# Optimization experiments

Measured on AMD Instinct MI355X. Metric: run time of the kernel, lower is better.

## Reference

```python
import jax, jax.numpy as jnp
import numpy as np

D_MODEL = 512
D_FF = 4 * D_MODEL
NUM_EXPERTS = 8
TOP_K = 2
NUM_TASKS = 16
D_TASK = 64
BATCH = 8
SEQ = 4096
LN_EPS = 1e-5


def setup_inputs() -> dict:
    key = jax.random.key(0)
    ks = jax.random.split(key, 10)
    s_in = 1.0 / np.sqrt(D_MODEL)
    s_ff = 1.0 / np.sqrt(D_FF)
    s_g = 1.0 / np.sqrt(D_MODEL + D_TASK)
    return {
        "x": jax.random.normal(ks[0], (BATCH, SEQ, D_MODEL), jnp.float32),
        "task_id": jax.random.randint(ks[1], (BATCH,), 0, NUM_TASKS),
        "w1": jax.random.normal(ks[2], (NUM_EXPERTS, D_MODEL, D_FF), jnp.float32) * s_in,
        "b1": jnp.zeros((NUM_EXPERTS, D_FF), jnp.float32),
        "w2": jax.random.normal(ks[3], (NUM_EXPERTS, D_FF, D_MODEL), jnp.float32) * s_ff,
        "b2": jnp.zeros((NUM_EXPERTS, D_MODEL), jnp.float32),
        "task_emb": jax.random.normal(ks[4], (NUM_TASKS, D_TASK), jnp.float32),
        "gate_w": jax.random.normal(ks[5], (D_MODEL + D_TASK, NUM_EXPERTS), jnp.float32) * s_g,
        "gate_b": jnp.zeros((NUM_EXPERTS,), jnp.float32),
    }


def reference(x, task_id, w1, b1, w2, b2, task_emb, gate_w, gate_b):
    B, S, D = x.shape
    E = w1.shape[0]

    # F.layer_norm(x, x.shape[1:]): normalize over (seq, d_model) jointly, no affine
    mean = jnp.mean(x, axis=(1, 2), keepdims=True)
    var = jnp.var(x, axis=(1, 2), keepdims=True)
    x_norm = (x - mean) * jax.lax.rsqrt(var + LN_EPS)

    t_emb = task_emb[task_id]                       # [B, d_task]
    t_emb = jnp.broadcast_to(t_emb[:, None, :], (B, S, t_emb.shape[-1]))
    gate_in = jnp.concatenate([x_norm, t_emb], axis=-1)
    logits = gate_in @ gate_w + gate_b              # [B, S, E]

    topk_logits, topk_idx = jax.lax.top_k(logits, TOP_K)   # [B, S, K]
    topk_probs = jax.nn.softmax(topk_logits, axis=-1)

    flat_x = x.reshape(-1, D)                       # [T, D]
    flat_idx = topk_idx.reshape(-1, TOP_K)          # [T, K]
    flat_p = topk_probs.reshape(-1, TOP_K)          # [T, K]

    assign = jax.nn.one_hot(flat_idx, E, dtype=x.dtype)    # [T, K, E]
    combine = jnp.einsum("tk,tke->te", flat_p, assign)     # [T, E] per-token expert weight

    out = jnp.zeros_like(flat_x)
    for e in range(E):  # fixed small expert loop
        h = jax.nn.silu(flat_x @ w1[e] + b1[e])
        y = h @ w2[e] + b2[e]
        out = out + y * combine[:, e:e + 1]
    final_output = out.reshape(B, S, D)

    usage = jnp.sum(assign, axis=(0, 1))            # [E] assignment counts
    usage_mean = jnp.mean(usage) + 1e-6
    usage_std = jnp.std(usage, ddof=1)              # torch.std is unbiased
    lb_loss = (usage_std / usage_mean) ** 2

    return final_output, lb_loss, topk_idx, task_id
```

## Files before the change

kernel.cpp:

```cpp
#include <hip/hip_runtime.h>

#define NB      8
#define SEQ     4096
#define DM      512
#define DFF     2048
#define NE      8
#define NTOK    32768
#define NPB     2097152
#define MAXROWS 66560
#define MAXTILES 520

#define OUT_LB   16777216
#define OUT_TOPK 16777217
#define OUT_TASK 16842753

#define WS_BSTATS   0
#define WS_DMEAN    8192
#define WS_DRSTD    8256
#define WS_DCOLSUM  8320
#define WS_DTASK    8384
#define WS_HIST     8896
#define WS_CURSOR   8928
#define WS_SEGOFF   8960
#define WS_HDR_END  9216
#define WS_ROUTE_E  9216
#define WS_ROUTE_P  271360
#define WS_ATOK     533504
#define WS_APROB    799744
#define WS_TOKPOS   1065984
#define WS_W1T      1328128
#define WS_W2T      18105344
#define WS_XB       34882560
#define WS_Y        68436992
#define WS_H        136594432

typedef __attribute__((ext_vector_type(4))) float  f32x4;
typedef __attribute__((ext_vector_type(8))) __bf16 bf16x8;
typedef __attribute__((ext_vector_type(8))) short  s16x8;

__device__ __forceinline__ unsigned short f2bf(float f) {
    unsigned int u = __builtin_bit_cast(unsigned int, f);
    u += 0x7FFFu + ((u >> 16) & 1u);
    return (unsigned short)(u >> 16);
}
__device__ __forceinline__ float bf2f(unsigned short b) {
    unsigned int u = ((unsigned int)b) << 16;
    return __builtin_bit_cast(float, u);
}
__device__ __forceinline__ unsigned int pkbf(float a, float b) {
    unsigned int r;
    asm("v_cvt_pk_bf16_f32 %0, %1, %2" : "=v"(r) : "v"(a), "v"(b));
    return r;
}

#define GLDS16(g, l)                                                              \
    __builtin_amdgcn_global_load_lds(                                             \
        (const __attribute__((address_space(1))) unsigned int*)(const void*)(g),  \
        (__attribute__((address_space(3))) unsigned int*)(void*)(l), 16, 0, 0)

__global__ void k_transpose_bf16(const float* __restrict__ in,
                                 unsigned short* __restrict__ outT,
                                 int R, int C) {
    __shared__ float tile[32][33];
    int e = blockIdx.z;
    const float* src = in + (size_t)e * R * C;
    unsigned short* dst = outT + (size_t)e * R * C;
    int tx = threadIdx.x & 31, ty = threadIdx.x >> 5;
    int c0 = blockIdx.x * 32, r0 = blockIdx.y * 32;
#pragma unroll
    for (int i = 0; i < 4; i++) {
        int r = r0 + ty + i * 8;
        tile[ty + i * 8][tx] = src[(size_t)r * C + c0 + tx];
    }
    __syncthreads();
#pragma unroll
    for (int i = 0; i < 4; i++) {
        int rr = c0 + ty + i * 8;
        dst[(size_t)rr * R + r0 + tx] = f2bf(tile[tx][ty + i * 8]);
    }
}

__global__ void k_xbf16(const float* __restrict__ x, unsigned short* __restrict__ xb) {
    size_t i = ((size_t)blockIdx.x * 256 + threadIdx.x) * 8;
    float4 a = *(const float4*)(x + i);
    float4 b = *(const float4*)(x + i + 4);
    s16x8 o = {(short)f2bf(a.x), (short)f2bf(a.y), (short)f2bf(a.z), (short)f2bf(a.w),
               (short)f2bf(b.x), (short)f2bf(b.y), (short)f2bf(b.z), (short)f2bf(b.w)};
    *(s16x8*)(xb + i) = o;
}

__global__ void k_reduce_stats(const float* __restrict__ x, double* __restrict__ bstats) {
    int b = blockIdx.y, c = blockIdx.x, t = threadIdx.x;
    const float* p = x + (size_t)b * NPB + (size_t)c * 32768;
    double s = 0.0, ss = 0.0;
#pragma unroll 4
    for (int i = 0; i < 32; i++) {
        float4 v = *(const float4*)(p + i * 1024 + t * 4);
        s  += (double)v.x + (double)v.y + (double)v.z + (double)v.w;
        ss += (double)v.x * v.x + (double)v.y * v.y + (double)v.z * v.z + (double)v.w * v.w;
    }
    for (int o = 32; o; o >>= 1) { s += __shfl_down(s, o); ss += __shfl_down(ss, o); }
    __shared__ double as_[4], ass_[4];
    int w = t >> 6;
    if ((t & 63) == 0) { as_[w] = s; ass_[w] = ss; }
    __syncthreads();
    if (t == 0) {
        s  = as_[0] + as_[1] + as_[2] + as_[3];
        ss = ass_[0] + ass_[1] + ass_[2] + ass_[3];
        bstats[(b * 64 + c) * 2]     = s;
        bstats[(b * 64 + c) * 2 + 1] = ss;
    }
}

__global__ void k_finalize(const double* __restrict__ bstats,
                           double* __restrict__ dmean, double* __restrict__ drstd,
                           double* __restrict__ dcolsum, double* __restrict__ dtask,
                           const float* __restrict__ gw, const float* __restrict__ gb,
                           const float* __restrict__ temb, const int* __restrict__ task_id,
                           float* __restrict__ out_task) {
    int t = threadIdx.x;
    int b = t >> 5, l = t & 31;
    double s  = bstats[(b * 64 + l) * 2]     + bstats[(b * 64 + l + 32) * 2];
    double ss = bstats[(b * 64 + l) * 2 + 1] + bstats[(b * 64 + l + 32) * 2 + 1];
    for (int o = 16; o; o >>= 1) { s += __shfl_down(s, o, 32); ss += __shfl_down(ss, o, 32); }
    if (l == 0) {
        double N = (double)NPB;
        double m = s / N;
        double var = ss / N - m * m;
        dmean[b] = m;
        drstd[b] = 1.0 / sqrt(var + 1e-5);
    }
    __shared__ double colp[32][8];
    {
        int e = t & 7, g = t >> 3;
        double a = 0.0;
        for (int r = g * 16; r < g * 16 + 16; r++) a += (double)gw[r * 8 + e];
        colp[g][e] = a;
    }
    __syncthreads();
    if (t < 8) {
        double a = 0.0;
        for (int g = 0; g < 32; g++) a += colp[g][t];
        dcolsum[t] = a;
    }
    if (t < 64) {
        int b2 = t >> 3, e = t & 7;
        int tid = task_id[b2];
        double a = (double)gb[e];
        for (int d = 0; d < 64; d++)
            a += (double)temb[tid * 64 + d] * (double)gw[(512 + d) * 8 + e];
        dtask[t] = a;
    }
    if (t < 8) out_task[t] = (float)task_id[t];
}

__global__ void __launch_bounds__(256) k_gate(const float* __restrict__ x,
                                              const float* __restrict__ gw,
                                              const double* __restrict__ dmean,
                                              const double* __restrict__ drstd,
                                              const double* __restrict__ dcolsum,
                                              const double* __restrict__ dtask,
                                              int* __restrict__ hist,
                                              int2* __restrict__ route_e,
                                              float2* __restrict__ route_p,
                                              float* __restrict__ out_topk) {
    __shared__ float gws[DM * 8];
    __shared__ int lh[8];
    int t = threadIdx.x;
    if (t < 8) lh[t] = 0;
#pragma unroll
    for (int i = 0; i < 16; i++) gws[i * 256 + t] = gw[i * 256 + t];
    __syncthreads();

    int token = blockIdx.x * 256 + t;
    int b = token >> 12;
    const float4* xp = (const float4*)(x + (size_t)token * DM);

    double acc[8] = {0, 0, 0, 0, 0, 0, 0, 0};
#pragma unroll 2
    for (int i = 0; i < 128; i++) {
        float4 v = xp[i];
        double dx = v.x, dy = v.y, dz = v.z, dw = v.w;
        const float* g = &gws[i * 32];
#pragma unroll
        for (int e = 0; e < 8; e++)
            acc[e] += dx * (double)g[e] + dy * (double)g[8 + e]
                    + dz * (double)g[16 + e] + dw * (double)g[24 + e];
    }

    double m = dmean[b], rs = drstd[b];
    double lg[8];
#pragma unroll
    for (int e = 0; e < 8; e++) lg[e] = rs * (acc[e] - m * dcolsum[e]) + dtask[b * 8 + e];
    int i0 = 0;
#pragma unroll
    for (int e = 1; e < 8; e++) if (lg[e] > lg[i0]) i0 = e;
    int i1 = (i0 == 0) ? 1 : 0;
#pragma unroll
    for (int e = 0; e < 8; e++) if (e != i0 && lg[e] > lg[i1]) i1 = e;
    double d = exp(lg[i1] - lg[i0]);
    double p0 = 1.0 / (1.0 + d);
    double p1 = d / (1.0 + d);
    out_topk[token * 2]     = (float)i0;
    out_topk[token * 2 + 1] = (float)i1;
    atomicAdd(&lh[i0], 1);
    atomicAdd(&lh[i1], 1);
    route_e[token] = make_int2(i0, i1);
    route_p[token] = make_float2((float)p0, (float)p1);
    __syncthreads();
    if (t < 8) atomicAdd(&hist[t], lh[t]);
}

__global__ void k_offsets_lb(const int* __restrict__ hist, int* __restrict__ seg_off,
                             float* __restrict__ out_lb) {
    if (threadIdx.x == 0) {
        int off = 0;
        double ssd = 0.0;
        for (int e = 0; e < 8; e++) {
            seg_off[e] = off;
            off += (hist[e] + 127) & ~127;
            double d = (double)hist[e] - 8192.0;
            ssd += d * d;
        }
        seg_off[8] = off;
        double stdv = sqrt(ssd / 7.0);
        double m = 8192.0 + 1e-6;
        double r = stdv / m;
        *out_lb = (float)(r * r);
    }
}

__global__ void __launch_bounds__(256) k_scatter(const int2* __restrict__ route_e,
                                                 const float2* __restrict__ route_p,
                                                 const int* __restrict__ seg_off,
                                                 int* __restrict__ cursor,
                                                 int* __restrict__ atok,
                                                 float* __restrict__ aprob,
                                                 int* __restrict__ tokpos) {
    __shared__ int lcount[8];
    __shared__ int lbase[8];
    int t = threadIdx.x;
    if (t < 8) lcount[t] = 0;
    __syncthreads();
    int tok = blockIdx.x * 256 + t;
    int2 e = route_e[tok];
    float2 p = route_p[tok];
    int p0 = atomicAdd(&lcount[e.x], 1);
    int p1 = atomicAdd(&lcount[e.y], 1);
    __syncthreads();
    if (t < 8) lbase[t] = atomicAdd(&cursor[t], lcount[t]);
    __syncthreads();
    int a0 = seg_off[e.x] + lbase[e.x] + p0;
    atok[a0] = tok; aprob[a0] = p.x;
    int a1 = seg_off[e.y] + lbase[e.y] + p1;
    atok[a1] = tok; aprob[a1] = p.y;
    tokpos[tok * 2]     = a0;
    tokpos[tok * 2 + 1] = a1;
}


__global__ void __launch_bounds__(256) k_gemm1(const unsigned short* __restrict__ xb,
                                               const unsigned short* __restrict__ w1t,
                                               const float* __restrict__ b1,
                                               const int* __restrict__ atok,
                                               const int* __restrict__ seg_off,
                                               unsigned short* __restrict__ H,
                                               int t0) {
    int nwg = (int)gridDim.x;
    int bid = (int)blockIdx.x;
    int wg = (bid & 7) * (nwg >> 3) + (bid >> 3);
    int xt = wg >> 4, y = wg & 15;
    int r0 = (t0 + xt) * 128;
    if (r0 >= seg_off[8]) return;
    int e = 0;
    while (seg_off[e + 1] <= r0) e++;
    int f0 = y * 128;

    int tid = threadIdx.x;
    int w = tid >> 6, l = tid & 63;
    int c = l & 7;

    __shared__ __align__(16) unsigned short As[2][128 * 64];
    __shared__ __align__(16) unsigned short Bs[2][128 * 64];

    const unsigned short* asrc[4];
    const unsigned short* bsrc[4];
    unsigned short*       adst[4];
    unsigned short*       bdst[4];
#pragma unroll
    for (int j = 0; j < 4; j++) {
        int R = w * 32 + j * 8 + (l >> 3);
        int cs = c ^ (R & 7);
        int tok = atok[r0 + R]; if (tok < 0) tok = 0;
        asrc[j] = xb + (size_t)tok * DM + cs * 8;
        bsrc[j] = w1t + ((size_t)e * DFF + f0 + R) * DM + cs * 8;
        adst[j] = &As[0][(size_t)(w * 32 + j * 8) * 64];
        bdst[j] = &Bs[0][(size_t)(w * 32 + j * 8) * 64];
    }

    f32x4 acc[4][4] = {};
    int wr = w >> 1, wc = w & 1, lr = l & 15, q = l >> 4;

#pragma unroll
    for (int j = 0; j < 4; j++) { GLDS16(asrc[j], adst[j]); GLDS16(bsrc[j], bdst[j]); }

    int cur = 0;
    for (int it = 0; it < DM / 64; ++it) {
        if (it + 1 < DM / 64) {
            int kn = (it + 1) * 64;
            int off = (cur ^ 1) * 128 * 64;
#pragma unroll
            for (int j = 0; j < 4; j++) {
                GLDS16(asrc[j] + kn, adst[j] + off);
                GLDS16(bsrc[j] + kn, bdst[j] + off);
            }
            asm volatile("s_waitcnt vmcnt(8)" ::: "memory");
        } else {
            asm volatile("s_waitcnt vmcnt(0)" ::: "memory");
        }
        __builtin_amdgcn_s_barrier();
        __builtin_amdgcn_sched_barrier(0);
        __builtin_amdgcn_s_setprio(1);
        const unsigned short* Ab = &As[cur][0];
        const unsigned short* Bb = &Bs[cur][0];
#pragma unroll
        for (int h = 0; h < 2; h++) {
            bf16x8 af[4], bfv[4];
#pragma unroll
            for (int m = 0; m < 4; m++) {
                int R = wr * 64 + m * 16 + lr;
                af[m] = *(const bf16x8*)&Ab[R * 64 + (((h << 2) + q) ^ (R & 7)) * 8];
            }
#pragma unroll
            for (int n = 0; n < 4; n++) {
                int R = wc * 64 + n * 16 + lr;
                bfv[n] = *(const bf16x8*)&Bb[R * 64 + (((h << 2) + q) ^ (R & 7)) * 8];
            }
#pragma unroll
            for (int m = 0; m < 4; m++)
#pragma unroll
                for (int n = 0; n < 4; n++)
                    acc[m][n] = __builtin_amdgcn_mfma_f32_16x16x32_bf16(bfv[n], af[m], acc[m][n], 0, 0, 0);
        }
        __builtin_amdgcn_s_setprio(0);
        __builtin_amdgcn_sched_barrier(0);
        asm volatile("" ::: "memory");
        __builtin_amdgcn_s_barrier();
        cur ^= 1;
    }

    const float* b1e = b1 + e * DFF + f0;
#pragma unroll
    for (int m = 0; m < 4; m++) {
        int r = wr * 64 + m * 16 + lr;
        unsigned short* hrow = H + ((size_t)xt * 128 + r) * DFF + f0;
#pragma unroll
        for (int n = 0; n < 4; n++) {
            int fc = wc * 64 + n * 16 + q * 4;
            float4 bias = *(const float4*)(b1e + fc);
            float v0 = acc[m][n][0] + bias.x; v0 = v0 / (1.0f + __expf(-v0));
            float v1 = acc[m][n][1] + bias.y; v1 = v1 / (1.0f + __expf(-v1));
            float v2 = acc[m][n][2] + bias.z; v2 = v2 / (1.0f + __expf(-v2));
            float v3 = acc[m][n][3] + bias.w; v3 = v3 / (1.0f + __expf(-v3));
            uint2 pk = make_uint2(pkbf(v0, v1), pkbf(v2, v3));
            *(uint2*)(hrow + fc) = pk;
        }
    }
}

__global__ void __launch_bounds__(256) k_gemm2(const unsigned short* __restrict__ H,
                                               const unsigned short* __restrict__ w2t,
                                               const int* __restrict__ seg_off,
                                               unsigned short* __restrict__ Y,
                                               int t0) {
    int nwg = (int)gridDim.x;
    int bid = (int)blockIdx.x;
    int wg = (bid & 7) * (nwg >> 3) + (bid >> 3);
    int xt = wg >> 2, y = wg & 3;
    int r0 = (t0 + xt) * 128;
    if (r0 >= seg_off[8]) return;
    int e = 0;
    while (seg_off[e + 1] <= r0) e++;
    int d0 = y * 128;

    int tid = threadIdx.x;
    int w = tid >> 6, l = tid & 63;
    int c = l & 7;

    __shared__ __align__(16) unsigned short As[2][128 * 64];
    __shared__ __align__(16) unsigned short Bs[2][128 * 64];

    const unsigned short* asrc[4];
    const unsigned short* bsrc[4];
    unsigned short*       adst[4];
    unsigned short*       bdst[4];
#pragma unroll
    for (int j = 0; j < 4; j++) {
        int R = w * 32 + j * 8 + (l >> 3);
        int cs = c ^ (R & 7);
        asrc[j] = H + ((size_t)xt * 128 + R) * DFF + cs * 8;
        bsrc[j] = w2t + ((size_t)e * DM + d0 + R) * DFF + cs * 8;
        adst[j] = &As[0][(size_t)(w * 32 + j * 8) * 64];
        bdst[j] = &Bs[0][(size_t)(w * 32 + j * 8) * 64];
    }

    f32x4 acc[4][4] = {};
    int wr = w >> 1, wc = w & 1, lr = l & 15, q = l >> 4;

#pragma unroll
    for (int j = 0; j < 4; j++) { GLDS16(asrc[j], adst[j]); GLDS16(bsrc[j], bdst[j]); }

    int cur = 0;
    for (int it = 0; it < DFF / 64; ++it) {
        if (it + 1 < DFF / 64) {
            int kn = (it + 1) * 64;
            int off = (cur ^ 1) * 128 * 64;
#pragma unroll
            for (int j = 0; j < 4; j++) {
                GLDS16(asrc[j] + kn, adst[j] + off);
                GLDS16(bsrc[j] + kn, bdst[j] + off);
            }
            asm volatile("s_waitcnt vmcnt(8)" ::: "memory");
        } else {
            asm volatile("s_waitcnt vmcnt(0)" ::: "memory");
        }
        __builtin_amdgcn_s_barrier();
        __builtin_amdgcn_sched_barrier(0);
        __builtin_amdgcn_s_setprio(1);
        const unsigned short* Ab = &As[cur][0];
        const unsigned short* Bb = &Bs[cur][0];
#pragma unroll
        for (int h = 0; h < 2; h++) {
            bf16x8 af[4], bfv[4];
#pragma unroll
            for (int m = 0; m < 4; m++) {
                int R = wr * 64 + m * 16 + lr;
                af[m] = *(const bf16x8*)&Ab[R * 64 + (((h << 2) + q) ^ (R & 7)) * 8];
            }
#pragma unroll
            for (int n = 0; n < 4; n++) {
                int R = wc * 64 + n * 16 + lr;
                bfv[n] = *(const bf16x8*)&Bb[R * 64 + (((h << 2) + q) ^ (R & 7)) * 8];
            }
#pragma unroll
            for (int m = 0; m < 4; m++)
#pragma unroll
                for (int n = 0; n < 4; n++)
                    acc[m][n] = __builtin_amdgcn_mfma_f32_16x16x32_bf16(bfv[n], af[m], acc[m][n], 0, 0, 0);
        }
        __builtin_amdgcn_s_setprio(0);
        __builtin_amdgcn_sched_barrier(0);
        asm volatile("" ::: "memory");
        __builtin_amdgcn_s_barrier();
        cur ^= 1;
    }

#pragma unroll
    for (int m = 0; m < 4; m++) {
        int r = wr * 64 + m * 16 + lr;
        unsigned short* yrow = Y + (size_t)(r0 + r) * DM + d0;
#pragma unroll
        for (int n = 0; n < 4; n++) {
            int dc = wc * 64 + n * 16 + q * 4;
            uint2 pk = make_uint2(pkbf(acc[m][n][0], acc[m][n][1]),
                                  pkbf(acc[m][n][2], acc[m][n][3]));
            *(uint2*)(yrow + dc) = pk;
        }
    }
}

__global__ void __launch_bounds__(256) k_combine(const unsigned short* __restrict__ Y,
                                                 const float* __restrict__ b2,
                                                 const int* __restrict__ tokpos,
                                                 const int2* __restrict__ route_e,
                                                 const float2* __restrict__ route_p,
                                                 float* __restrict__ out) {
    int gt = blockIdx.x * 256 + threadIdx.x;
    int token = gt >> 6;
    int cbase = (gt & 63) * 8;
    int2 e = route_e[token];
    float2 p = route_p[token];
    int a0 = tokpos[token * 2], a1 = tokpos[token * 2 + 1];
    s16x8 y0 = *(const s16x8*)(Y + (size_t)a0 * DM + cbase);
    s16x8 y1 = *(const s16x8*)(Y + (size_t)a1 * DM + cbase);
    const float4* bb0 = (const float4*)(b2 + e.x * DM + cbase);
    const float4* bb1 = (const float4*)(b2 + e.y * DM + cbase);
    float4 b00 = bb0[0], b01 = bb0[1];
    float4 b10 = bb1[0], b11 = bb1[1];
    float r[8];
    r[0] = p.x * (bf2f((unsigned short)y0[0]) + b00.x) + p.y * (bf2f((unsigned short)y1[0]) + b10.x);
    r[1] = p.x * (bf2f((unsigned short)y0[1]) + b00.y) + p.y * (bf2f((unsigned short)y1[1]) + b10.y);
    r[2] = p.x * (bf2f((unsigned short)y0[2]) + b00.z) + p.y * (bf2f((unsigned short)y1[2]) + b10.z);
    r[3] = p.x * (bf2f((unsigned short)y0[3]) + b00.w) + p.y * (bf2f((unsigned short)y1[3]) + b10.w);
    r[4] = p.x * (bf2f((unsigned short)y0[4]) + b01.x) + p.y * (bf2f((unsigned short)y1[4]) + b11.x);
    r[5] = p.x * (bf2f((unsigned short)y0[5]) + b01.y) + p.y * (bf2f((unsigned short)y1[5]) + b11.y);
    r[6] = p.x * (bf2f((unsigned short)y0[6]) + b01.z) + p.y * (bf2f((unsigned short)y1[6]) + b11.z);
    r[7] = p.x * (bf2f((unsigned short)y0[7]) + b01.w) + p.y * (bf2f((unsigned short)y1[7]) + b11.w);
    float* op = out + (size_t)token * DM + cbase;
    *(float4*)op       = make_float4(r[0], r[1], r[2], r[3]);
    *(float4*)(op + 4) = make_float4(r[4], r[5], r[6], r[7]);
}

extern "C" void kernel_launch(void* const* d_in, const int* in_sizes, int n_in,
                              void* d_out, int out_size, void* d_ws, size_t ws_size,
                              hipStream_t stream) {
    const float* x       = (const float*)d_in[0];
    const int*   task_id = (const int*)d_in[1];
    const float* w1      = (const float*)d_in[2];
    const float* b1      = (const float*)d_in[3];
    const float* w2      = (const float*)d_in[4];
    const float* b2      = (const float*)d_in[5];
    const float* temb    = (const float*)d_in[6];
    const float* gw      = (const float*)d_in[7];
    const float* gb      = (const float*)d_in[8];
    float* out = (float*)d_out;

    char* ws = (char*)d_ws;
    double* bstats   = (double*)(ws + WS_BSTATS);
    double* dmean    = (double*)(ws + WS_DMEAN);
    double* drstd    = (double*)(ws + WS_DRSTD);
    double* dcolsum  = (double*)(ws + WS_DCOLSUM);
    double* dtask    = (double*)(ws + WS_DTASK);
    int*    hist     = (int*)(ws + WS_HIST);
    int*    cursor   = (int*)(ws + WS_CURSOR);
    int*    seg_off  = (int*)(ws + WS_SEGOFF);
    int2*   route_e  = (int2*)(ws + WS_ROUTE_E);
    float2* route_p  = (float2*)(ws + WS_ROUTE_P);
    int*    atok     = (int*)(ws + WS_ATOK);
    float*  aprob    = (float*)(ws + WS_APROB);
    int*    tokpos   = (int*)(ws + WS_TOKPOS);
    unsigned short* w1t = (unsigned short*)(ws + WS_W1T);
    unsigned short* w2t = (unsigned short*)(ws + WS_W2T);
    unsigned short* xb  = (unsigned short*)(ws + WS_XB);
    unsigned short* Y   = (unsigned short*)(ws + WS_Y);
    unsigned short* H   = (unsigned short*)(ws + WS_H);

    int TPC = (int)((ws_size - (size_t)WS_H) / (size_t)(128 * DFF * 2));
    if (TPC > MAXTILES) TPC = MAXTILES;
    TPC &= ~1;
    if (TPC < 2) TPC = 2;

    hipMemsetAsync(ws, 0, WS_HDR_END, stream);
    hipMemsetAsync(ws + WS_ATOK, 0xFF, (size_t)MAXROWS * sizeof(int), stream);

    k_transpose_bf16<<<dim3(DFF / 32, DM / 32, NE), 256, 0, stream>>>(w1, w1t, DM, DFF);
    k_transpose_bf16<<<dim3(DM / 32, DFF / 32, NE), 256, 0, stream>>>(w2, w2t, DFF, DM);
    k_xbf16<<<NTOK * DM / 8 / 256, 256, 0, stream>>>(x, xb);

    k_reduce_stats<<<dim3(64, NB), 256, 0, stream>>>(x, bstats);
    k_finalize<<<1, 256, 0, stream>>>(bstats, dmean, drstd, dcolsum, dtask,
                                      gw, gb, temb, task_id, out + OUT_TASK);

    k_gate<<<NTOK / 256, 256, 0, stream>>>(x, gw, dmean, drstd, dcolsum, dtask,
                                           hist, route_e, route_p, out + OUT_TOPK);
    k_offsets_lb<<<1, 64, 0, stream>>>(hist, seg_off, out + OUT_LB);
    k_scatter<<<NTOK / 256, 256, 0, stream>>>(route_e, route_p, seg_off, cursor,
                                              atok, aprob, tokpos);

    for (int t0 = 0; t0 < MAXTILES; t0 += TPC) {
        k_gemm1<<<TPC * 16, 256, 0, stream>>>(xb, w1t, b1, atok, seg_off, H, t0);
        k_gemm2<<<TPC * 4, 256, 0, stream>>>(H, w2t, seg_off, Y, t0);
    }
    k_combine<<<NTOK / 4, 256, 0, stream>>>(Y, b2, tokpos, route_e, route_p, out);
}
```

Baseline: 642.4 us.

## Use 256x256 GEMM tiles with 512 threads and fuse x stats with bf16 cast

Both expert GEMMs now use 256x256 output tiles with 8 waves per block, 128 KiB of LDS and a prefetch two k-steps ahead. The larger tiles raise operand reuse and cut the number of global loads per FLOP, at the cost of higher register pressure, one block per CU and more padding per expert (segments rounded to 256 rows). Separately, the x-to-bf16 cast and the layer-norm sum/sumsq reduction are fused into one pass over x, producing 1024 partials per batch that finalize now reduces.

```diff
diff --git a/kernel.cpp b/kernel.cpp
--- a/kernel.cpp
+++ b/kernel.cpp
@@ -7,32 +7,32 @@
 #define NE      8
 #define NTOK    32768
 #define NPB     2097152
-#define MAXROWS 66560
-#define MAXTILES 520
+#define MAXROWS 67584
+#define MAXT256 264
 
 #define OUT_LB   16777216
 #define OUT_TOPK 16777217
 #define OUT_TASK 16842753
 
 #define WS_BSTATS   0
-#define WS_DMEAN    8192
-#define WS_DRSTD    8256
-#define WS_DCOLSUM  8320
-#define WS_DTASK    8384
-#define WS_HIST     8896
-#define WS_CURSOR   8928
-#define WS_SEGOFF   8960
-#define WS_HDR_END  9216
-#define WS_ROUTE_E  9216
-#define WS_ROUTE_P  271360
-#define WS_ATOK     533504
-#define WS_APROB    799744
-#define WS_TOKPOS   1065984
-#define WS_W1T      1328128
-#define WS_W2T      18105344
-#define WS_XB       34882560
-#define WS_Y        68436992
-#define WS_H        136594432
+#define WS_DMEAN    131072
+#define WS_DRSTD    131136
+#define WS_DCOLSUM  131200
+#define WS_DTASK    131264
+#define WS_HIST     131776
+#define WS_CURSOR   131808
+#define WS_SEGOFF   131840
+#define WS_HDR_END  131904
+#define WS_ROUTE_E  131904
+#define WS_ROUTE_P  394048
+#define WS_ATOK     656192
+#define WS_APROB    926528
+#define WS_TOKPOS   1196864
+#define WS_W1T      1459008
+#define WS_W2T      18236224
+#define WS_XB       35013440
+#define WS_Y        68567872
+#define WS_H        137773888
 
 typedef __attribute__((ext_vector_type(4))) float  f32x4;
 typedef __attribute__((ext_vector_type(8))) __bf16 bf16x8;
@@ -80,26 +80,21 @@
     }
 }
 
-__global__ void k_xbf16(const float* __restrict__ x, unsigned short* __restrict__ xb) {
-    size_t i = ((size_t)blockIdx.x * 256 + threadIdx.x) * 8;
-    float4 a = *(const float4*)(x + i);
-    float4 b = *(const float4*)(x + i + 4);
+__global__ void __launch_bounds__(256) k_xstats(const float* __restrict__ x,
+                                                unsigned short* __restrict__ xb,
+                                                double* __restrict__ bstats) {
+    int b = blockIdx.y, cblk = blockIdx.x, t = threadIdx.x;
+    size_t base = (size_t)b * NPB + (size_t)cblk * 2048 + (size_t)t * 8;
+    float4 a = *(const float4*)(x + base);
+    float4 v = *(const float4*)(x + base + 4);
     s16x8 o = {(short)f2bf(a.x), (short)f2bf(a.y), (short)f2bf(a.z), (short)f2bf(a.w),
-               (short)f2bf(b.x), (short)f2bf(b.y), (short)f2bf(b.z), (short)f2bf(b.w)};
-    *(s16x8*)(xb + i) = o;
-}
-
-__global__ void k_reduce_stats(const float* __restrict__ x, double* __restrict__ bstats) {
-    int b = blockIdx.y, c = blockIdx.x, t = threadIdx.x;
-    const float* p = x + (size_t)b * NPB + (size_t)c * 32768;
-    double s = 0.0, ss = 0.0;
-#pragma unroll 4
-    for (int i = 0; i < 32; i++) {
-        float4 v = *(const float4*)(p + i * 1024 + t * 4);
-        s  += (double)v.x + (double)v.y + (double)v.z + (double)v.w;
-        ss += (double)v.x * v.x + (double)v.y * v.y + (double)v.z * v.z + (double)v.w * v.w;
-    }
-    for (int o = 32; o; o >>= 1) { s += __shfl_down(s, o); ss += __shfl_down(ss, o); }
+               (short)f2bf(v.x), (short)f2bf(v.y), (short)f2bf(v.z), (short)f2bf(v.w)};
+    *(s16x8*)(xb + base) = o;
+    double s  = (double)a.x + (double)a.y + (double)a.z + (double)a.w
+              + (double)v.x + (double)v.y + (double)v.z + (double)v.w;
+    double ss = (double)a.x * a.x + (double)a.y * a.y + (double)a.z * a.z + (double)a.w * a.w
+              + (double)v.x * v.x + (double)v.y * v.y + (double)v.z * v.z + (double)v.w * v.w;
+    for (int o2 = 32; o2; o2 >>= 1) { s += __shfl_down(s, o2); ss += __shfl_down(ss, o2); }
     __shared__ double as_[4], ass_[4];
     int w = t >> 6;
     if ((t & 63) == 0) { as_[w] = s; ass_[w] = ss; }
@@ -107,8 +102,8 @@
     if (t == 0) {
         s  = as_[0] + as_[1] + as_[2] + as_[3];
         ss = ass_[0] + ass_[1] + ass_[2] + ass_[3];
-        bstats[(b * 64 + c) * 2]     = s;
-        bstats[(b * 64 + c) * 2 + 1] = ss;
+        bstats[(b * 1024 + cblk) * 2]     = s;
+        bstats[(b * 1024 + cblk) * 2 + 1] = ss;
     }
 }
 
@@ -120,8 +115,11 @@
                            float* __restrict__ out_task) {
     int t = threadIdx.x;
     int b = t >> 5, l = t & 31;
-    double s  = bstats[(b * 64 + l) * 2]     + bstats[(b * 64 + l + 32) * 2];
-    double ss = bstats[(b * 64 + l) * 2 + 1] + bstats[(b * 64 + l + 32) * 2 + 1];
+    double s = 0.0, ss = 0.0;
+    for (int i = l; i < 1024; i += 32) {
+        s  += bstats[(b * 1024 + i) * 2];
+        ss += bstats[(b * 1024 + i) * 2 + 1];
+    }
     for (int o = 16; o; o >>= 1) { s += __shfl_down(s, o, 32); ss += __shfl_down(ss, o, 32); }
     if (l == 0) {
         double N = (double)NPB;
@@ -218,7 +216,7 @@
         double ssd = 0.0;
         for (int e = 0; e < 8; e++) {
             seg_off[e] = off;
-            off += (hist[e] + 127) & ~127;
+            off += (hist[e] + 255) & ~255;
             double d = (double)hist[e] - 8192.0;
             ssd += d * d;
         }
@@ -259,29 +257,29 @@
 }
 
 
-__global__ void __launch_bounds__(256) k_gemm1(const unsigned short* __restrict__ xb,
-                                               const unsigned short* __restrict__ w1t,
-                                               const float* __restrict__ b1,
-                                               const int* __restrict__ atok,
-                                               const int* __restrict__ seg_off,
-                                               unsigned short* __restrict__ H,
-                                               int t0) {
+__global__ void __launch_bounds__(512, 1) k_gemm1(const unsigned short* __restrict__ xb,
+                                                  const unsigned short* __restrict__ w1t,
+                                                  const float* __restrict__ b1,
+                                                  const int* __restrict__ atok,
+                                                  const int* __restrict__ seg_off,
+                                                  unsigned short* __restrict__ H,
+                                                  int t0) {
     int nwg = (int)gridDim.x;
     int bid = (int)blockIdx.x;
     int wg = (bid & 7) * (nwg >> 3) + (bid >> 3);
-    int xt = wg >> 4, y = wg & 15;
-    int r0 = (t0 + xt) * 128;
+    int xt = wg >> 3, y = wg & 7;
+    int r0 = (t0 + xt) * 256;
     if (r0 >= seg_off[8]) return;
     int e = 0;
     while (seg_off[e + 1] <= r0) e++;
-    int f0 = y * 128;
+    int f0 = y * 256;
 
     int tid = threadIdx.x;
     int w = tid >> 6, l = tid & 63;
     int c = l & 7;
 
-    __shared__ __align__(16) unsigned short As[2][128 * 64];
-    __shared__ __align__(16) unsigned short Bs[2][128 * 64];
+    __shared__ __align__(16) unsigned short As[2 * 256 * 64];
+    __shared__ __align__(16) unsigned short Bs[2 * 256 * 64];
 
     const unsigned short* asrc[4];
     const unsigned short* bsrc[4];
@@ -289,26 +287,54 @@
     unsigned short*       bdst[4];
 #pragma unroll
     for (int j = 0; j < 4; j++) {
-        int R = w * 32 + j * 8 + (l >> 3);
-        int cs = c ^ (R & 7);
-        int tok = atok[r0 + R]; if (tok < 0) tok = 0;
+        int row = j * 64 + w * 8 + (l >> 3);
+        int cs = c ^ (row & 7);
+        int tok = atok[r0 + row]; if (tok < 0) tok = 0;
         asrc[j] = xb + (size_t)tok * DM + cs * 8;
-        bsrc[j] = w1t + ((size_t)e * DFF + f0 + R) * DM + cs * 8;
-        adst[j] = &As[0][(size_t)(w * 32 + j * 8) * 64];
-        bdst[j] = &Bs[0][(size_t)(w * 32 + j * 8) * 64];
-    }
-
-    f32x4 acc[4][4] = {};
-    int wr = w >> 1, wc = w & 1, lr = l & 15, q = l >> 4;
-
+        bsrc[j] = w1t + ((size_t)e * DFF + f0 + row) * DM + cs * 8;
+        adst[j] = &As[(j * 64 + w * 8) * 64];
+        bdst[j] = &Bs[(j * 64 + w * 8) * 64];
+    }
+
+    f32x4 acc[8][4] = {};
+    int wr = w >> 2, wc = w & 3, lr = l & 15, q = l >> 4;
+
+    const int NK = DM / 64;
 #pragma unroll
     for (int j = 0; j < 4; j++) { GLDS16(asrc[j], adst[j]); GLDS16(bsrc[j], bdst[j]); }
-
-    int cur = 0;
-    for (int it = 0; it < DM / 64; ++it) {
-        if (it + 1 < DM / 64) {
-            int kn = (it + 1) * 64;
-            int off = (cur ^ 1) * 128 * 64;
+#pragma unroll
+    for (int j = 0; j < 4; j++) { GLDS16(asrc[j] + 64, adst[j] + 16384); GLDS16(bsrc[j] + 64, bdst[j] + 16384); }
+    asm volatile("s_waitcnt vmcnt(8)" ::: "memory");
+    __builtin_amdgcn_s_barrier();
+
+    for (int kt = 0; kt < NK; ++kt) {
+        const unsigned short* Ab = &As[(kt & 1) * 16384];
+        const unsigned short* Bb = &Bs[(kt & 1) * 16384];
+        __builtin_amdgcn_s_setprio(1);
+#pragma unroll
+        for (int ks = 0; ks < 2; ks++) {
+            bf16x8 bfv[4];
+#pragma unroll
+            for (int n = 0; n < 4; n++) {
+                int R = wc * 64 + n * 16 + lr;
+                bfv[n] = *(const bf16x8*)&Bb[R * 64 + (((ks << 2) + q) ^ (R & 7)) * 8];
+            }
+#pragma unroll
+            for (int m = 0; m < 8; m++) {
+                int R = wr * 128 + m * 16 + lr;
+                bf16x8 af = *(const bf16x8*)&Ab[R * 64 + (((ks << 2) + q) ^ (R & 7)) * 8];
+#pragma unroll
+                for (int n = 0; n < 4; n++)
+                    acc[m][n] = __builtin_amdgcn_mfma_f32_16x16x32_bf16(bfv[n], af, acc[m][n], 0, 0, 0);
+            }
+        }
+        __builtin_amdgcn_s_setprio(0);
+        __builtin_amdgcn_sched_barrier(0);
+        asm volatile("" ::: "memory");
+        __builtin_amdgcn_s_barrier();
+        if (kt + 2 < NK) {
+            int kn = (kt + 2) * 64;
+            int off = (kt & 1) * 16384;
 #pragma unroll
             for (int j = 0; j < 4; j++) {
                 GLDS16(asrc[j] + kn, adst[j] + off);
@@ -320,40 +346,13 @@
         }
         __builtin_amdgcn_s_barrier();
         __builtin_amdgcn_sched_barrier(0);
-        __builtin_amdgcn_s_setprio(1);
-        const unsigned short* Ab = &As[cur][0];
-        const unsigned short* Bb = &Bs[cur][0];
-#pragma unroll
-        for (int h = 0; h < 2; h++) {
-            bf16x8 af[4], bfv[4];
-#pragma unroll
-            for (int m = 0; m < 4; m++) {
-                int R = wr * 64 + m * 16 + lr;
-                af[m] = *(const bf16x8*)&Ab[R * 64 + (((h << 2) + q) ^ (R & 7)) * 8];
-            }
-#pragma unroll
-            for (int n = 0; n < 4; n++) {
-                int R = wc * 64 + n * 16 + lr;
-                bfv[n] = *(const bf16x8*)&Bb[R * 64 + (((h << 2) + q) ^ (R & 7)) * 8];
-            }
-#pragma unroll
-            for (int m = 0; m < 4; m++)
-#pragma unroll
-                for (int n = 0; n < 4; n++)
-                    acc[m][n] = __builtin_amdgcn_mfma_f32_16x16x32_bf16(bfv[n], af[m], acc[m][n], 0, 0, 0);
-        }
-        __builtin_amdgcn_s_setprio(0);
-        __builtin_amdgcn_sched_barrier(0);
-        asm volatile("" ::: "memory");
-        __builtin_amdgcn_s_barrier();
-        cur ^= 1;
     }
 
     const float* b1e = b1 + e * DFF + f0;
 #pragma unroll
-    for (int m = 0; m < 4; m++) {
-        int r = wr * 64 + m * 16 + lr;
-        unsigned short* hrow = H + ((size_t)xt * 128 + r) * DFF + f0;
+    for (int m = 0; m < 8; m++) {
+        int r = wr * 128 + m * 16 + lr;
+        unsigned short* hrow = H + ((size_t)xt * 256 + r) * DFF + f0;
 #pragma unroll
         for (int n = 0; n < 4; n++) {
             int fc = wc * 64 + n * 16 + q * 4;
@@ -362,33 +361,32 @@
             float v1 = acc[m][n][1] + bias.y; v1 = v1 / (1.0f + __expf(-v1));
             float v2 = acc[m][n][2] + bias.z; v2 = v2 / (1.0f + __expf(-v2));
             float v3 = acc[m][n][3] + bias.w; v3 = v3 / (1.0f + __expf(-v3));
-            uint2 pk = make_uint2(pkbf(v0, v1), pkbf(v2, v3));
-            *(uint2*)(hrow + fc) = pk;
-        }
-    }
-}
-
-__global__ void __launch_bounds__(256) k_gemm2(const unsigned short* __restrict__ H,
-                                               const unsigned short* __restrict__ w2t,
-                                               const int* __restrict__ seg_off,
-                                               unsigned short* __restrict__ Y,
-                                               int t0) {
+            *(uint2*)(hrow + fc) = make_uint2(pkbf(v0, v1), pkbf(v2, v3));
+        }
+    }
+}
+
+__global__ void __launch_bounds__(512, 1) k_gemm2(const unsigned short* __restrict__ H,
+                                                  const unsigned short* __restrict__ w2t,
+                                                  const int* __restrict__ seg_off,
+                                                  unsigned short* __restrict__ Y,
+                                                  int t0) {
     int nwg = (int)gridDim.x;
     int bid = (int)blockIdx.x;
     int wg = (bid & 7) * (nwg >> 3) + (bid >> 3);
-    int xt = wg >> 2, y = wg & 3;
-    int r0 = (t0 + xt) * 128;
+    int xt = wg >> 1, y = wg & 1;
+    int r0 = (t0 + xt) * 256;
     if (r0 >= seg_off[8]) return;
     int e = 0;
     while (seg_off[e + 1] <= r0) e++;
-    int d0 = y * 128;
+    int d0 = y * 256;
 
     int tid = threadIdx.x;
     int w = tid >> 6, l = tid & 63;
     int c = l & 7;
 
-    __shared__ __align__(16) unsigned short As[2][128 * 64];
-    __shared__ __align__(16) unsigned short Bs[2][128 * 64];
+    __shared__ __align__(16) unsigned short As[2 * 256 * 64];
+    __shared__ __align__(16) unsigned short Bs[2 * 256 * 64];
 
     const unsigned short* asrc[4];
     const unsigned short* bsrc[4];
@@ -396,25 +394,53 @@
     unsigned short*       bdst[4];
 #pragma unroll
     for (int j = 0; j < 4; j++) {
-        int R = w * 32 + j * 8 + (l >> 3);
-        int cs = c ^ (R & 7);
-        asrc[j] = H + ((size_t)xt * 128 + R) * DFF + cs * 8;
-        bsrc[j] = w2t + ((size_t)e * DM + d0 + R) * DFF + cs * 8;
-        adst[j] = &As[0][(size_t)(w * 32 + j * 8) * 64];
-        bdst[j] = &Bs[0][(size_t)(w * 32 + j * 8) * 64];
-    }
-
-    f32x4 acc[4][4] = {};
-    int wr = w >> 1, wc = w & 1, lr = l & 15, q = l >> 4;
-
+        int row = j * 64 + w * 8 + (l >> 3);
+        int cs = c ^ (row & 7);
+        asrc[j] = H + ((size_t)xt * 256 + row) * DFF + cs * 8;
+        bsrc[j] = w2t + ((size_t)e * DM + d0 + row) * DFF + cs * 8;
+        adst[j] = &As[(j * 64 + w * 8) * 64];
+        bdst[j] = &Bs[(j * 64 + w * 8) * 64];
+    }
+
+    f32x4 acc[8][4] = {};
+    int wr = w >> 2, wc = w & 3, lr = l & 15, q = l >> 4;
+
+    const int NK = DFF / 64;
 #pragma unroll
     for (int j = 0; j < 4; j++) { GLDS16(asrc[j], adst[j]); GLDS16(bsrc[j], bdst[j]); }
-
-    int cur = 0;
-    for (int it = 0; it < DFF / 64; ++it) {
-        if (it + 1 < DFF / 64) {
-            int kn = (it + 1) * 64;
-            int off = (cur ^ 1) * 128 * 64;
+#pragma unroll
+    for (int j = 0; j < 4; j++) { GLDS16(asrc[j] + 64, adst[j] + 16384); GLDS16(bsrc[j] + 64, bdst[j] + 16384); }
+    asm volatile("s_waitcnt vmcnt(8)" ::: "memory");
+    __builtin_amdgcn_s_barrier();
+
+    for (int kt = 0; kt < NK; ++kt) {
+        const unsigned short* Ab = &As[(kt & 1) * 16384];
+        const unsigned short* Bb = &Bs[(kt & 1) * 16384];
+        __builtin_amdgcn_s_setprio(1);
+#pragma unroll
+        for (int ks = 0; ks < 2; ks++) {
+            bf16x8 bfv[4];
+#pragma unroll
+            for (int n = 0; n < 4; n++) {
+                int R = wc * 64 + n * 16 + lr;
+                bfv[n] = *(const bf16x8*)&Bb[R * 64 + (((ks << 2) + q) ^ (R & 7)) * 8];
+            }
+#pragma unroll
+            for (int m = 0; m < 8; m++) {
+                int R = wr * 128 + m * 16 + lr;
+                bf16x8 af = *(const bf16x8*)&Ab[R * 64 + (((ks << 2) + q) ^ (R & 7)) * 8];
+#pragma unroll
+                for (int n = 0; n < 4; n++)
+                    acc[m][n] = __builtin_amdgcn_mfma_f32_16x16x32_bf16(bfv[n], af, acc[m][n], 0, 0, 0);
+            }
+        }
+        __builtin_amdgcn_s_setprio(0);
+        __builtin_amdgcn_sched_barrier(0);
+        asm volatile("" ::: "memory");
+        __builtin_amdgcn_s_barrier();
+        if (kt + 2 < NK) {
+            int kn = (kt + 2) * 64;
+            int off = (kt & 1) * 16384;
 #pragma unroll
             for (int j = 0; j < 4; j++) {
                 GLDS16(asrc[j] + kn, adst[j] + off);
@@ -426,45 +452,17 @@
         }
         __builtin_amdgcn_s_barrier();
         __builtin_amdgcn_sched_barrier(0);
-        __builtin_amdgcn_s_setprio(1);
-        const unsigned short* Ab = &As[cur][0];
-        const unsigned short* Bb = &Bs[cur][0];
-#pragma unroll
-        for (int h = 0; h < 2; h++) {
-            bf16x8 af[4], bfv[4];
-#pragma unroll
-            for (int m = 0; m < 4; m++) {
-                int R = wr * 64 + m * 16 + lr;
-                af[m] = *(const bf16x8*)&Ab[R * 64 + (((h << 2) + q) ^ (R & 7)) * 8];
-            }
-#pragma unroll
-            for (int n = 0; n < 4; n++) {
-                int R = wc * 64 + n * 16 + lr;
-                bfv[n] = *(const bf16x8*)&Bb[R * 64 + (((h << 2) + q) ^ (R & 7)) * 8];
-            }
-#pragma unroll
-            for (int m = 0; m < 4; m++)
-#pragma unroll
-                for (int n = 0; n < 4; n++)
-                    acc[m][n] = __builtin_amdgcn_mfma_f32_16x16x32_bf16(bfv[n], af[m], acc[m][n], 0, 0, 0);
-        }
-        __builtin_amdgcn_s_setprio(0);
-        __builtin_amdgcn_sched_barrier(0);
-        asm volatile("" ::: "memory");
-        __builtin_amdgcn_s_barrier();
-        cur ^= 1;
-    }
-
-#pragma unroll
-    for (int m = 0; m < 4; m++) {
-        int r = wr * 64 + m * 16 + lr;
+    }
+
+#pragma unroll
+    for (int m = 0; m < 8; m++) {
+        int r = wr * 128 + m * 16 + lr;
         unsigned short* yrow = Y + (size_t)(r0 + r) * DM + d0;
 #pragma unroll
         for (int n = 0; n < 4; n++) {
             int dc = wc * 64 + n * 16 + q * 4;
-            uint2 pk = make_uint2(pkbf(acc[m][n][0], acc[m][n][1]),
-                                  pkbf(acc[m][n][2], acc[m][n][3]));
-            *(uint2*)(yrow + dc) = pk;
+            *(uint2*)(yrow + dc) = make_uint2(pkbf(acc[m][n][0], acc[m][n][1]),
+                                              pkbf(acc[m][n][2], acc[m][n][3]));
         }
     }
 }
@@ -535,19 +533,18 @@
     unsigned short* Y   = (unsigned short*)(ws + WS_Y);
     unsigned short* H   = (unsigned short*)(ws + WS_H);
 
-    int TPC = (int)((ws_size - (size_t)WS_H) / (size_t)(128 * DFF * 2));
-    if (TPC > MAXTILES) TPC = MAXTILES;
-    TPC &= ~1;
-    if (TPC < 2) TPC = 2;
+    int TPC = (int)((ws_size - (size_t)WS_H) / (size_t)(256 * DFF * 2));
+    if (TPC > 132) TPC = 132;
+    TPC &= ~3;
+    if (TPC < 4) TPC = 4;
 
     hipMemsetAsync(ws, 0, WS_HDR_END, stream);
     hipMemsetAsync(ws + WS_ATOK, 0xFF, (size_t)MAXROWS * sizeof(int), stream);
 
     k_transpose_bf16<<<dim3(DFF / 32, DM / 32, NE), 256, 0, stream>>>(w1, w1t, DM, DFF);
     k_transpose_bf16<<<dim3(DM / 32, DFF / 32, NE), 256, 0, stream>>>(w2, w2t, DFF, DM);
-    k_xbf16<<<NTOK * DM / 8 / 256, 256, 0, stream>>>(x, xb);
-
-    k_reduce_stats<<<dim3(64, NB), 256, 0, stream>>>(x, bstats);
+
+    k_xstats<<<dim3(1024, NB), 256, 0, stream>>>(x, xb, bstats);
     k_finalize<<<1, 256, 0, stream>>>(bstats, dmean, drstd, dcolsum, dtask,
                                       gw, gb, temb, task_id, out + OUT_TASK);
 
@@ -557,9 +554,9 @@
     k_scatter<<<NTOK / 256, 256, 0, stream>>>(route_e, route_p, seg_off, cursor,
                                               atok, aprob, tokpos);
 
-    for (int t0 = 0; t0 < MAXTILES; t0 += TPC) {
-        k_gemm1<<<TPC * 16, 256, 0, stream>>>(xb, w1t, b1, atok, seg_off, H, t0);
-        k_gemm2<<<TPC * 4, 256, 0, stream>>>(H, w2t, seg_off, Y, t0);
+    for (int t0 = 0; t0 < MAXT256; t0 += TPC) {
+        k_gemm1<<<TPC * 8, 512, 0, stream>>>(xb, w1t, b1, atok, seg_off, H, t0);
+        k_gemm2<<<TPC * 2, 512, 0, stream>>>(H, w2t, seg_off, Y, t0);
     }
     k_combine<<<NTOK / 4, 256, 0, stream>>>(Y, b2, tokpos, route_e, route_p, out);
 }
```

Result: slower. 781.4 us (+21.6%).

## Fuse bf16 cast, LN stats and raw gate dot into one pass over x

Applied to the files above, without the earlier changes.

Merges the x-to-bf16 conversion, per-batch sum/sumsq reduction and the raw gate projection into a single kernel, so x (64 MB fp32) is read once instead of three times. The gate dot products are stored as raw doubles and a light k_topk kernel applies mean/rstd correction after finalize. It also rebalances the GEMM chunk size so the tiles split evenly across launches. The cost is a token-per-thread access pattern for the bf16 conversion (strided, less coalesced) plus an extra 2 MB raw buffer.

```diff
diff --git a/kernel.cpp b/kernel.cpp
--- a/kernel.cpp
+++ b/kernel.cpp
@@ -15,24 +15,25 @@
 #define OUT_TASK 16842753
 
 #define WS_BSTATS   0
-#define WS_DMEAN    8192
-#define WS_DRSTD    8256
-#define WS_DCOLSUM  8320
-#define WS_DTASK    8384
-#define WS_HIST     8896
-#define WS_CURSOR   8928
-#define WS_SEGOFF   8960
-#define WS_HDR_END  9216
-#define WS_ROUTE_E  9216
-#define WS_ROUTE_P  271360
-#define WS_ATOK     533504
-#define WS_APROB    799744
-#define WS_TOKPOS   1065984
-#define WS_W1T      1328128
-#define WS_W2T      18105344
-#define WS_XB       34882560
-#define WS_Y        68436992
-#define WS_H        136594432
+#define WS_DMEAN    2048
+#define WS_DRSTD    2112
+#define WS_DCOLSUM  2176
+#define WS_DTASK    2240
+#define WS_HIST     2752
+#define WS_CURSOR   2784
+#define WS_SEGOFF   2816
+#define WS_HDR_END  2944
+#define WS_ROUTE_E  2944
+#define WS_ROUTE_P  265088
+#define WS_ATOK     527232
+#define WS_APROB    793472
+#define WS_TOKPOS   1059712
+#define WS_RAW      1321856
+#define WS_W1T      3419008
+#define WS_W2T      20196224
+#define WS_XB       36973440
+#define WS_Y        70527872
+#define WS_H        138685312
 
 typedef __attribute__((ext_vector_type(4))) float  f32x4;
 typedef __attribute__((ext_vector_type(8))) __bf16 bf16x8;
@@ -80,25 +81,54 @@
     }
 }
 
-__global__ void k_xbf16(const float* __restrict__ x, unsigned short* __restrict__ xb) {
-    size_t i = ((size_t)blockIdx.x * 256 + threadIdx.x) * 8;
-    float4 a = *(const float4*)(x + i);
-    float4 b = *(const float4*)(x + i + 4);
-    s16x8 o = {(short)f2bf(a.x), (short)f2bf(a.y), (short)f2bf(a.z), (short)f2bf(a.w),
-               (short)f2bf(b.x), (short)f2bf(b.y), (short)f2bf(b.z), (short)f2bf(b.w)};
-    *(s16x8*)(xb + i) = o;
-}
-
-__global__ void k_reduce_stats(const float* __restrict__ x, double* __restrict__ bstats) {
-    int b = blockIdx.y, c = blockIdx.x, t = threadIdx.x;
-    const float* p = x + (size_t)b * NPB + (size_t)c * 32768;
+__global__ void __launch_bounds__(256) k_xgate(const float* __restrict__ x,
+                                               const float* __restrict__ gw,
+                                               unsigned short* __restrict__ xb,
+                                               double* __restrict__ bstats,
+                                               double* __restrict__ raw) {
+    __shared__ float gws[DM * 8];
+    int t = threadIdx.x;
+#pragma unroll
+    for (int i = 0; i < 16; i++) gws[i * 256 + t] = gw[i * 256 + t];
+    __syncthreads();
+
+    int token = blockIdx.x * 256 + t;
+    const float4* xp = (const float4*)(x + (size_t)token * DM);
+    unsigned short* xbp = xb + (size_t)token * DM;
+
+    double acc[8] = {0, 0, 0, 0, 0, 0, 0, 0};
     double s = 0.0, ss = 0.0;
-#pragma unroll 4
-    for (int i = 0; i < 32; i++) {
-        float4 v = *(const float4*)(p + i * 1024 + t * 4);
-        s  += (double)v.x + (double)v.y + (double)v.z + (double)v.w;
-        ss += (double)v.x * v.x + (double)v.y * v.y + (double)v.z * v.z + (double)v.w * v.w;
-    }
+#pragma unroll 2
+    for (int i = 0; i < 128; i += 2) {
+        float4 v0 = xp[i];
+        float4 v1 = xp[i + 1];
+        {
+            double dx = v0.x, dy = v0.y, dz = v0.z, dw = v0.w;
+            const float* g = &gws[i * 32];
+#pragma unroll
+            for (int e = 0; e < 8; e++)
+                acc[e] += dx * (double)g[e] + dy * (double)g[8 + e]
+                        + dz * (double)g[16 + e] + dw * (double)g[24 + e];
+            s  += dx + dy + dz + dw;
+            ss += dx * dx + dy * dy + dz * dz + dw * dw;
+        }
+        {
+            double dx = v1.x, dy = v1.y, dz = v1.z, dw = v1.w;
+            const float* g = &gws[(i + 1) * 32];
+#pragma unroll
+            for (int e = 0; e < 8; e++)
+                acc[e] += dx * (double)g[e] + dy * (double)g[8 + e]
+                        + dz * (double)g[16 + e] + dw * (double)g[24 + e];
+            s  += dx + dy + dz + dw;
+            ss += dx * dx + dy * dy + dz * dz + dw * dw;
+        }
+        s16x8 o = {(short)f2bf(v0.x), (short)f2bf(v0.y), (short)f2bf(v0.z), (short)f2bf(v0.w),
+                   (short)f2bf(v1.x), (short)f2bf(v1.y), (short)f2bf(v1.z), (short)f2bf(v1.w)};
+        *(s16x8*)(xbp + i * 4) = o;
+    }
+#pragma unroll
+    for (int e = 0; e < 8; e++) raw[(size_t)token * 8 + e] = acc[e];
+
     for (int o = 32; o; o >>= 1) { s += __shfl_down(s, o); ss += __shfl_down(ss, o); }
     __shared__ double as_[4], ass_[4];
     int w = t >> 6;
@@ -107,8 +137,8 @@
     if (t == 0) {
         s  = as_[0] + as_[1] + as_[2] + as_[3];
         ss = ass_[0] + ass_[1] + ass_[2] + ass_[3];
-        bstats[(b * 64 + c) * 2]     = s;
-        bstats[(b * 64 + c) * 2 + 1] = ss;
+        bstats[blockIdx.x * 2]     = s;
+        bstats[blockIdx.x * 2 + 1] = ss;
     }
 }
 
@@ -119,16 +149,17 @@
                            const float* __restrict__ temb, const int* __restrict__ task_id,
                            float* __restrict__ out_task) {
     int t = threadIdx.x;
-    int b = t >> 5, l = t & 31;
-    double s  = bstats[(b * 64 + l) * 2]     + bstats[(b * 64 + l + 32) * 2];
-    double ss = bstats[(b * 64 + l) * 2 + 1] + bstats[(b * 64 + l + 32) * 2 + 1];
-    for (int o = 16; o; o >>= 1) { s += __shfl_down(s, o, 32); ss += __shfl_down(ss, o, 32); }
-    if (l == 0) {
+    if (t < 8) {
+        double s = 0.0, ss = 0.0;
+        for (int i = 0; i < 16; i++) {
+            s  += bstats[(t * 16 + i) * 2];
+            ss += bstats[(t * 16 + i) * 2 + 1];
+        }
         double N = (double)NPB;
         double m = s / N;
         double var = ss / N - m * m;
-        dmean[b] = m;
-        drstd[b] = 1.0 / sqrt(var + 1e-5);
+        dmean[t] = m;
+        drstd[t] = 1.0 / sqrt(var + 1e-5);
     }
     __shared__ double colp[32][8];
     {
@@ -154,8 +185,7 @@
     if (t < 8) out_task[t] = (float)task_id[t];
 }
 
-__global__ void __launch_bounds__(256) k_gate(const float* __restrict__ x,
-                                              const float* __restrict__ gw,
+__global__ void __launch_bounds__(256) k_topk(const double* __restrict__ raw,
                                               const double* __restrict__ dmean,
                                               const double* __restrict__ drstd,
                                               const double* __restrict__ dcolsum,
@@ -164,34 +194,17 @@
                                               int2* __restrict__ route_e,
                                               float2* __restrict__ route_p,
                                               float* __restrict__ out_topk) {
-    __shared__ float gws[DM * 8];
     __shared__ int lh[8];
     int t = threadIdx.x;
     if (t < 8) lh[t] = 0;
-#pragma unroll
-    for (int i = 0; i < 16; i++) gws[i * 256 + t] = gw[i * 256 + t];
-    __syncthreads();
-
+    __syncthreads();
     int token = blockIdx.x * 256 + t;
     int b = token >> 12;
-    const float4* xp = (const float4*)(x + (size_t)token * DM);
-
-    double acc[8] = {0, 0, 0, 0, 0, 0, 0, 0};
-#pragma unroll 2
-    for (int i = 0; i < 128; i++) {
-        float4 v = xp[i];
-        double dx = v.x, dy = v.y, dz = v.z, dw = v.w;
-        const float* g = &gws[i * 32];
-#pragma unroll
-        for (int e = 0; e < 8; e++)
-            acc[e] += dx * (double)g[e] + dy * (double)g[8 + e]
-                    + dz * (double)g[16 + e] + dw * (double)g[24 + e];
-    }
-
     double m = dmean[b], rs = drstd[b];
     double lg[8];
 #pragma unroll
-    for (int e = 0; e < 8; e++) lg[e] = rs * (acc[e] - m * dcolsum[e]) + dtask[b * 8 + e];
+    for (int e = 0; e < 8; e++)
+        lg[e] = rs * (raw[(size_t)token * 8 + e] - m * dcolsum[e]) + dtask[b * 8 + e];
     int i0 = 0;
 #pragma unroll
     for (int e = 1; e < 8; e++) if (lg[e] > lg[i0]) i0 = e;
@@ -362,8 +375,7 @@
             float v1 = acc[m][n][1] + bias.y; v1 = v1 / (1.0f + __expf(-v1));
             float v2 = acc[m][n][2] + bias.z; v2 = v2 / (1.0f + __expf(-v2));
             float v3 = acc[m][n][3] + bias.w; v3 = v3 / (1.0f + __expf(-v3));
-            uint2 pk = make_uint2(pkbf(v0, v1), pkbf(v2, v3));
-            *(uint2*)(hrow + fc) = pk;
+            *(uint2*)(hrow + fc) = make_uint2(pkbf(v0, v1), pkbf(v2, v3));
         }
     }
 }
@@ -462,9 +474,8 @@
 #pragma unroll
         for (int n = 0; n < 4; n++) {
             int dc = wc * 64 + n * 16 + q * 4;
-            uint2 pk = make_uint2(pkbf(acc[m][n][0], acc[m][n][1]),
-                                  pkbf(acc[m][n][2], acc[m][n][3]));
-            *(uint2*)(yrow + dc) = pk;
+            *(uint2*)(yrow + dc) = make_uint2(pkbf(acc[m][n][0], acc[m][n][1]),
+                                              pkbf(acc[m][n][2], acc[m][n][3]));
         }
     }
 }
@@ -529,6 +540,7 @@
     int*    atok     = (int*)(ws + WS_ATOK);
     float*  aprob    = (float*)(ws + WS_APROB);
     int*    tokpos   = (int*)(ws + WS_TOKPOS);
+    double* raw      = (double*)(ws + WS_RAW);
     unsigned short* w1t = (unsigned short*)(ws + WS_W1T);
     unsigned short* w2t = (unsigned short*)(ws + WS_W2T);
     unsigned short* xb  = (unsigned short*)(ws + WS_XB);
@@ -539,19 +551,23 @@
     if (TPC > MAXTILES) TPC = MAXTILES;
     TPC &= ~1;
     if (TPC < 2) TPC = 2;
+    {
+        int nch = (MAXTILES + TPC - 1) / TPC;
+        int bal = (MAXTILES + nch - 1) / nch;
+        bal = (bal + 1) & ~1;
+        if (bal <= TPC) TPC = bal;
+    }
 
     hipMemsetAsync(ws, 0, WS_HDR_END, stream);
     hipMemsetAsync(ws + WS_ATOK, 0xFF, (size_t)MAXROWS * sizeof(int), stream);
 
     k_transpose_bf16<<<dim3(DFF / 32, DM / 32, NE), 256, 0, stream>>>(w1, w1t, DM, DFF);
     k_transpose_bf16<<<dim3(DM / 32, DFF / 32, NE), 256, 0, stream>>>(w2, w2t, DFF, DM);
-    k_xbf16<<<NTOK * DM / 8 / 256, 256, 0, stream>>>(x, xb);
-
-    k_reduce_stats<<<dim3(64, NB), 256, 0, stream>>>(x, bstats);
+
+    k_xgate<<<NTOK / 256, 256, 0, stream>>>(x, gw, xb, bstats, raw);
     k_finalize<<<1, 256, 0, stream>>>(bstats, dmean, drstd, dcolsum, dtask,
                                       gw, gb, temb, task_id, out + OUT_TASK);
-
-    k_gate<<<NTOK / 256, 256, 0, stream>>>(x, gw, dmean, drstd, dcolsum, dtask,
+    k_topk<<<NTOK / 256, 256, 0, stream>>>(raw, dmean, drstd, dcolsum, dtask,
                                            hist, route_e, route_p, out + OUT_TOPK);
     k_offsets_lb<<<1, 64, 0, stream>>>(hist, seg_off, out + OUT_LB);
     k_scatter<<<NTOK / 256, 256, 0, stream>>>(route_e, route_p, seg_off, cursor,
```

New measurement: 565.0 us. -12.0%, faster.
